# Optimization experiments

Hardware: AMD Instinct MI355X
Metric: run time of the kernel (lower is better)

The kernel has to match this reference:

```python
import jax, jax.numpy as jnp
import numpy as np

N_NODES = 200000
N_EDGES = 3200000
N_FEAT = 165


def setup_inputs() -> dict:
    key = jax.random.key(0)
    ks = jax.random.split(key, 8)

    def glorot(k, fan_in, fan_out):
        lim = np.sqrt(6.0 / (fan_in + fan_out)).astype(np.float32)
        return jax.random.uniform(k, (fan_in, fan_out), jnp.float32, -lim, lim)

    x = jax.random.normal(ks[0], (N_NODES, N_FEAT), jnp.float32)
    edge_index = jax.random.randint(ks[1], (2, N_EDGES), 0, N_NODES, dtype=jnp.int64)
    return {
        "x": x,
        "edge_index": edge_index,
        "W1": glorot(ks[2], N_FEAT, 64), "b1": jnp.zeros((64,), jnp.float32),
        "W2": glorot(ks[3], 64, 16),     "b2": jnp.zeros((16,), jnp.float32),
        "W3": glorot(ks[4], 16, 2),      "b3": jnp.zeros((2,), jnp.float32),
    }


def _gcn_layer(x, src, dst, norm, W, b, n_nodes):
    # linear transform first (feature dim shrinks), then normalized scatter-add
    h = x @ W                                # [N, out]
    msg = h[src] * norm[:, None]             # gather over edges (incl. self-loops)
    out = jax.ops.segment_sum(msg, dst, num_segments=n_nodes)
    return out + b


def reference(x, edge_index, W1, b1, W2, b2, W3, b3):
    n = x.shape[0]
    loops = jnp.arange(n, dtype=edge_index.dtype)
    src = jnp.concatenate([edge_index[0], loops])   # PyG GCNConv adds self-loops
    dst = jnp.concatenate([edge_index[1], loops])
    # symmetric normalization deg^{-1/2}[src] * deg^{-1/2}[dst]
    deg = jax.ops.segment_sum(jnp.ones_like(dst, dtype=x.dtype), dst, num_segments=n)
    dinv = jnp.where(deg > 0, jax.lax.rsqrt(deg), 0.0)
    norm = dinv[src] * dinv[dst]                    # [E + N]

    h = jax.nn.relu(_gcn_layer(x, src, dst, norm, W1, b1, n))
    h = jax.nn.relu(_gcn_layer(h, src, dst, norm, W2, b2, n))
    h = _gcn_layer(h, src, dst, norm, W3, b3, n)
    return jax.nn.log_softmax(h, axis=1)
```

## Files before the change

### kernel.cpp

```cpp
#include <hip/hip_runtime.h>
#include <cstdint>
#include <math.h>

#define BLK 256
#define NBUK_MAX 1024

__device__ __forceinline__ float bf_lo(unsigned p) { return __uint_as_float(p << 16); }
__device__ __forceinline__ float bf_hi(unsigned p) { return __uint_as_float(p & 0xffff0000u); }
__device__ __forceinline__ unsigned pack2(float a, float b) {
  unsigned ua = __float_as_uint(a), ub = __float_as_uint(b);
  ua = (ua + 0x7fffu + ((ua >> 16) & 1u)) >> 16;
  ub = (ub + 0x7fffu + ((ub >> 16) & 1u)) >> 16;
  return (ua & 0xffffu) | (ub << 16);
}


__global__ void k_zero(int* __restrict__ p, int n) {
  int i = blockIdx.x * blockDim.x + threadIdx.x;
  if (i < n) p[i] = 0;
}


__global__ __launch_bounds__(BLK)
void k_bcount(const int* __restrict__ edges, long long E, long long chunk, int nbuk,
              int* __restrict__ bucket_counts) {
  __shared__ int hist[NBUK_MAX];
  for (int i = threadIdx.x; i < nbuk; i += BLK) hist[i] = 0;
  __syncthreads();
  long long beg = (long long)blockIdx.x * chunk;
  long long end = beg + chunk < E ? beg + chunk : E;
  for (long long e = beg + threadIdx.x; e < end; e += BLK)
    atomicAdd(&hist[edges[E + e] >> 8], 1);
  __syncthreads();
  for (int i = threadIdx.x; i < nbuk; i += BLK)
    if (hist[i]) atomicAdd(&bucket_counts[i], hist[i]);
}

__global__ __launch_bounds__(1024)
void k_bscan(const int* __restrict__ bucket_counts, int nbuk,
             int* __restrict__ bucket_start, int* __restrict__ bucket_cursor) {
  __shared__ int tmp[1024];
  int i = threadIdx.x;
  int v = (i < nbuk) ? bucket_counts[i] : 0;
  tmp[i] = v;
  __syncthreads();
  for (int off = 1; off < 1024; off <<= 1) {
    int t = (i >= off) ? tmp[i - off] : 0;
    __syncthreads();
    tmp[i] += t;
    __syncthreads();
  }
  if (i < nbuk) {
    int ex = tmp[i] - v;
    bucket_start[i] = ex;
    bucket_cursor[i] = ex;
  }
  if (i == nbuk - 1) bucket_start[nbuk] = tmp[i];
}

__global__ __launch_bounds__(BLK)
void k_bscatter(const int* __restrict__ edges, long long E, long long chunk, int nbuk,
                int* __restrict__ bucket_cursor, int* __restrict__ tmp_out) {
  __shared__ int hist[NBUK_MAX];
  __shared__ int base[NBUK_MAX];
  for (int i = threadIdx.x; i < nbuk; i += BLK) hist[i] = 0;
  __syncthreads();
  long long beg = (long long)blockIdx.x * chunk;
  long long end = beg + chunk < E ? beg + chunk : E;
  for (long long e = beg + threadIdx.x; e < end; e += BLK)
    atomicAdd(&hist[edges[E + e] >> 8], 1);
  __syncthreads();
  for (int i = threadIdx.x; i < nbuk; i += BLK) {
    int c = hist[i];
    base[i] = c ? atomicAdd(&bucket_cursor[i], c) : 0;
    hist[i] = 0;
  }
  __syncthreads();
  for (long long e = beg + threadIdx.x; e < end; e += BLK) {
    int s = edges[e];
    int d = edges[E + e];
    int b = d >> 8;
    int r = atomicAdd(&hist[b], 1);
    tmp_out[base[b] + r] = (s << 8) | (d & 255);
  }
}

__global__ __launch_bounds__(BLK)
void k_bfinal(const int* __restrict__ tmp_in, const int* __restrict__ bucket_start, int n,
              int* __restrict__ row_start, int* __restrict__ counts,
              float* __restrict__ dinv, int* __restrict__ col) {
  __shared__ int cnt[256];
  __shared__ int scan[256];
  __shared__ int cur[256];
  const int b = blockIdx.x, t = threadIdx.x;
  const int seg0 = bucket_start[b], seg1 = bucket_start[b + 1];
  cnt[t] = 0;
  __syncthreads();
  for (int i = seg0 + t; i < seg1; i += BLK) atomicAdd(&cnt[tmp_in[i] & 255], 1);
  __syncthreads();
  int v0 = cnt[t];
  scan[t] = v0;
  __syncthreads();
  for (int off = 1; off < 256; off <<= 1) {
    int x = (t >= off) ? scan[t - off] : 0;
    __syncthreads();
    scan[t] += x;
    __syncthreads();
  }
  int loff = scan[t] - v0;
  int v = b * 256 + t;
  if (v < n) {
    row_start[v] = seg0 + loff;
    counts[v] = v0;
    dinv[v] = rsqrtf((float)v0 + 1.0f);
  }
  cur[t] = loff;
  __syncthreads();
  for (int i = seg0 + t; i < seg1; i += BLK) {
    int p = tmp_in[i];
    int r = atomicAdd(&cur[p & 255], 1);
    col[seg0 + r] = p >> 8;
  }
}


#define XSTR 260

__global__ __launch_bounds__(BLK)
void k_gemm1(const float* __restrict__ in, const float* __restrict__ W,
             const float* __restrict__ dinv, unsigned* __restrict__ hs1, int n) {
  __shared__ float Xt[33 * XSTR];
  __shared__ float Wl[33 * 64];
  const int t = threadIdx.x;
  const int v0 = blockIdx.x * 256;
  const int tx = t & 7;
  const int ty = t >> 3;

  float xf[33];
  float wf[9];

  float acc[8][8];
#pragma unroll
  for (int i = 0; i < 8; ++i)
#pragma unroll
    for (int j = 0; j < 8; ++j) acc[i][j] = 0.f;

#pragma unroll
  for (int i = 0; i < 33; ++i) {
    int e = t + i * 256;
    int row = e / 33, c = e - row * 33;
    int v = v0 + row;
    xf[i] = (v < n) ? in[(size_t)v * 165 + c] : 0.f;
  }
#pragma unroll
  for (int i = 0; i < 9; ++i) {
    int e = t + i * 256;
    wf[i] = (e < 2112) ? W[e] : 0.f;
  }

  for (int kc = 0; kc < 165; kc += 33) {
    __syncthreads();
#pragma unroll
    for (int i = 0; i < 33; ++i) {
      int e = t + i * 256;
      int row = e / 33, c = e - row * 33;
      Xt[c * XSTR + row] = xf[i];
    }
#pragma unroll
    for (int i = 0; i < 9; ++i) {
      int e = t + i * 256;
      if (e < 2112) Wl[e] = wf[i];
    }
    __syncthreads();

    if (kc + 33 < 165) {
      int kn = kc + 33;
#pragma unroll
      for (int i = 0; i < 33; ++i) {
        int e = t + i * 256;
        int row = e / 33, c = e - row * 33;
        int v = v0 + row;
        xf[i] = (v < n) ? in[(size_t)v * 165 + kn + c] : 0.f;
      }
#pragma unroll
      for (int i = 0; i < 9; ++i) {
        int e = t + i * 256;
        wf[i] = (e < 2112) ? W[kn * 64 + e] : 0.f;
      }
    }

    for (int k = 0; k < 33; ++k) {
      const float4 xa = *(const float4*)&Xt[k * XSTR + ty * 8];
      const float4 xb = *(const float4*)&Xt[k * XSTR + ty * 8 + 4];
      const float4 wa = *(const float4*)&Wl[k * 64 + tx * 8];
      const float4 wb = *(const float4*)&Wl[k * 64 + tx * 8 + 4];
      const float xm[8] = {xa.x, xa.y, xa.z, xa.w, xb.x, xb.y, xb.z, xb.w};
      const float wc[8] = {wa.x, wa.y, wa.z, wa.w, wb.x, wb.y, wb.z, wb.w};
#pragma unroll
      for (int mi = 0; mi < 8; ++mi)
#pragma unroll
        for (int ci = 0; ci < 8; ++ci)
          acc[mi][ci] = fmaf(xm[mi], wc[ci], acc[mi][ci]);
    }
  }

#pragma unroll
  for (int mi = 0; mi < 8; ++mi) {
    int v = v0 + ty * 8 + mi;
    if (v < n) {
      float dv = dinv[v];
      uint4 r;
      r.x = pack2(acc[mi][0] * dv, acc[mi][1] * dv);
      r.y = pack2(acc[mi][2] * dv, acc[mi][3] * dv);
      r.z = pack2(acc[mi][4] * dv, acc[mi][5] * dv);
      r.w = pack2(acc[mi][6] * dv, acc[mi][7] * dv);
      ((uint4*)(hs1 + (size_t)v * 32))[tx] = r;
    }
  }
}


__global__ __launch_bounds__(BLK)
void k_gather64g2(const unsigned* __restrict__ hs1, const int* __restrict__ row_start,
                  const int* __restrict__ counts, const int* __restrict__ col,
                  const float* __restrict__ dinv, const float* __restrict__ b1,
                  const float* __restrict__ W2, unsigned* __restrict__ hs2, int n) {
  __shared__ float W2l[64 * 16];
  for (int i = threadIdx.x; i < 64 * 16; i += BLK) W2l[i] = W2[i];
  __syncthreads();

  int wave = threadIdx.x >> 6, lane = threadIdx.x & 63;
  int v = blockIdx.x * 4 + wave;
  if (v >= n) return;
  int sub = lane >> 5, u = lane & 31;
  int beg = row_start[v], cnt = counts[v];

  float a0, a1;
  if (sub == 0) {
    unsigned p = hs1[(size_t)v * 32 + u];
    a0 = bf_lo(p); a1 = bf_hi(p);
  } else {
    a0 = 0.f; a1 = 0.f;
  }

  int e = sub;
  for (; e + 6 < cnt; e += 8) {
    int s0 = col[beg + e];
    int s1 = col[beg + e + 2];
    int s2 = col[beg + e + 4];
    int s3 = col[beg + e + 6];
    unsigned p0 = hs1[(size_t)s0 * 32 + u];
    unsigned p1 = hs1[(size_t)s1 * 32 + u];
    unsigned p2 = hs1[(size_t)s2 * 32 + u];
    unsigned p3 = hs1[(size_t)s3 * 32 + u];
    a0 += (bf_lo(p0) + bf_lo(p1)) + (bf_lo(p2) + bf_lo(p3));
    a1 += (bf_hi(p0) + bf_hi(p1)) + (bf_hi(p2) + bf_hi(p3));
  }
  for (; e < cnt; e += 2) {
    unsigned p = hs1[(size_t)col[beg + e] * 32 + u];
    a0 += bf_lo(p); a1 += bf_hi(p);
  }
  a0 += __shfl_xor(a0, 32);
  a1 += __shfl_xor(a1, 32);

  float dv = dinv[v];
  float2 bb = ((const float2*)b1)[u];
  float r0 = fmaxf(fmaf(a0, dv, bb.x), 0.f);
  float r1 = fmaxf(fmaf(a1, dv, bb.y), 0.f);

  int o = lane & 15, q = lane >> 4;
  float part = 0.f;
#pragma unroll
  for (int i = 0; i < 16; i += 2) {
    int k = q * 16 + i;
    float e0 = __shfl(r0, k >> 1);
    float e1 = __shfl(r1, k >> 1);
    part = fmaf(e0, W2l[k * 16 + o], part);
    part = fmaf(e1, W2l[(k + 1) * 16 + o], part);
  }
  part += __shfl_xor(part, 16);
  part += __shfl_xor(part, 32);
  float h = part * dv;
  float hnext = __shfl_xor(h, 1);
  if (lane < 16 && (lane & 1) == 0)
    hs2[(size_t)v * 8 + (o >> 1)] = pack2(h, hnext);
}


__global__ __launch_bounds__(BLK)
void k_gather16g3(const unsigned* __restrict__ hs2, const int* __restrict__ row_start,
                  const int* __restrict__ counts, const int* __restrict__ col,
                  const float* __restrict__ dinv, const float* __restrict__ b2,
                  const float* __restrict__ W3, float* __restrict__ hs3, int n) {
  int wave = threadIdx.x >> 6, lane = threadIdx.x & 63;
  int v = blockIdx.x * 4 + wave;
  if (v >= n) return;
  int j = lane >> 3, p = lane & 7;
  int beg = row_start[v], cnt = counts[v];

  float a0 = 0.f, a1 = 0.f;
  int e = j;
  for (; e + 8 < cnt; e += 16) {
    unsigned pk0 = hs2[(size_t)col[beg + e] * 8 + p];
    unsigned pk1 = hs2[(size_t)col[beg + e + 8] * 8 + p];
    a0 += bf_lo(pk0) + bf_lo(pk1);
    a1 += bf_hi(pk0) + bf_hi(pk1);
  }
  if (e < cnt) {
    unsigned pk = hs2[(size_t)col[beg + e] * 8 + p];
    a0 += bf_lo(pk); a1 += bf_hi(pk);
  }
  a0 += __shfl_xor(a0, 8);  a1 += __shfl_xor(a1, 8);
  a0 += __shfl_xor(a0, 16); a1 += __shfl_xor(a1, 16);
  a0 += __shfl_xor(a0, 32); a1 += __shfl_xor(a1, 32);

  unsigned ps = hs2[(size_t)v * 8 + p];
  a0 += bf_lo(ps); a1 += bf_hi(ps);

  float dv = dinv[v];
  float2 bb = ((const float2*)b2)[p];
  float r0 = fmaxf(fmaf(a0, dv, bb.x), 0.f);
  float r1 = fmaxf(fmaf(a1, dv, bb.y), 0.f);

  int o = lane & 1;
  float part = 0.f;
#pragma unroll
  for (int i = 0; i < 8; ++i) {
    float e0 = __shfl(r0, i);
    float e1 = __shfl(r1, i);
    part = fmaf(e0, W3[(2 * i) * 2 + o], part);
    part = fmaf(e1, W3[(2 * i + 1) * 2 + o], part);
  }
  if (lane < 2) hs3[(size_t)v * 2 + o] = part * dv;
}


__global__ void k_gather2_lsm(const float* __restrict__ hs3, const int* __restrict__ row_start,
                              const int* __restrict__ counts, const int* __restrict__ col,
                              const float* __restrict__ dinv, const float* __restrict__ b,
                              float* __restrict__ out, int n) {
  int v = blockIdx.x * blockDim.x + threadIdx.x;
  if (v >= n) return;
  const float2* hs2v = (const float2*)hs3;
  int beg = row_start[v], cnt = counts[v];
  float2 self = hs2v[v];
  float a0 = self.x, a1 = self.y;
  for (int e = 0; e < cnt; ++e) {
    float2 m = hs2v[col[beg + e]];
    a0 += m.x;
    a1 += m.y;
  }
  float dv = dinv[v];
  a0 = fmaf(a0, dv, b[0]);
  a1 = fmaf(a1, dv, b[1]);
  float m = fmaxf(a0, a1);
  float l = m + logf(expf(a0 - m) + expf(a1 - m));
  out[2 * v] = a0 - l;
  out[2 * v + 1] = a1 - l;
}


extern "C" void kernel_launch(void* const* d_in, const int* in_sizes, int n_in,
                              void* d_out, int out_size, void* d_ws, size_t ws_size,
                              hipStream_t stream) {
  const float* x = (const float*)d_in[0];
  const int* edges = (const int*)d_in[1];
  const float* W1 = (const float*)d_in[2];
  const float* b1 = (const float*)d_in[3];
  const float* W2 = (const float*)d_in[4];
  const float* b2 = (const float*)d_in[5];
  const float* W3 = (const float*)d_in[6];
  const float* b3 = (const float*)d_in[7];
  float* out = (float*)d_out;

  const int N = in_sizes[0] / 165;
  const long long E = in_sizes[1] / 2;
  const int nbuk = (N + 255) >> 8;

  char* w = (char*)d_ws;
  int* counts        = (int*)w;  w += (size_t)N * 4;
  int* row_start     = (int*)w;  w += (size_t)N * 4;
  float* dinv        = (float*)w; w += (size_t)N * 4;
  int* bucket_counts = (int*)w;  w += (NBUK_MAX + 4) * 4;
  int* bucket_start  = (int*)w;  w += (NBUK_MAX + 4) * 4;
  int* bucket_cursor = (int*)w;  w += (NBUK_MAX + 4) * 4;
  int* col           = (int*)w;  w += (size_t)E * 4;
  unsigned* hs1      = (unsigned*)w; w += (size_t)N * 32 * 4;
  unsigned* hs2      = (unsigned*)w; w += (size_t)N * 8 * 4;
  float* hs3         = (float*)w;
  int* tmp = (int*)hs1;

  const int gN = (N + BLK - 1) / BLK;
  const int gW = (N + 3) / 4;
  const int NB_PART = 256;
  const long long chunk = (E + NB_PART - 1) / NB_PART;

  k_zero<<<(nbuk + BLK - 1) / BLK, BLK, 0, stream>>>(bucket_counts, nbuk);
  k_bcount<<<NB_PART, BLK, 0, stream>>>(edges, E, chunk, nbuk, bucket_counts);
  k_bscan<<<1, 1024, 0, stream>>>(bucket_counts, nbuk, bucket_start, bucket_cursor);
  k_bscatter<<<NB_PART, BLK, 0, stream>>>(edges, E, chunk, nbuk, bucket_cursor, tmp);
  k_bfinal<<<nbuk, BLK, 0, stream>>>(tmp, bucket_start, N, row_start, counts, dinv, col);

  k_gemm1<<<gN, BLK, 0, stream>>>(x, W1, dinv, hs1, N);

  k_gather64g2<<<gW, BLK, 0, stream>>>(hs1, row_start, counts, col, dinv, b1, W2, hs2, N);

  k_gather16g3<<<gW, BLK, 0, stream>>>(hs2, row_start, counts, col, dinv, b2, W3, hs3, N);

  k_gather2_lsm<<<gN, BLK, 0, stream>>>(hs3, row_start, counts, col, dinv, b3, out, N);
}
```

Baseline: 673.6 us.

## Rewrite first-layer GEMM with fp16 MFMA matrix instructions

Replaces the FP32 register-tiled shared-memory GEMM for X@W1 with a wave-level MFMA 16x16x32 fp16 kernel. W1 is pre-swizzled into LDS as half8 fragments, and X rows are loaded directly from global memory and converted to fp16 per fragment. The aim is to move the 165x64 matmul onto the matrix cores and drop the X transpose staging. It gives up precision (fp16 inputs) and uses uncoalesced 8-float row loads from the stride-165 input. The dinv float4 read may go past n on the last block.

```diff
diff --git a/kernel.cpp b/kernel.cpp
--- a/kernel.cpp
+++ b/kernel.cpp
@@ -13,6 +13,9 @@
   ub = (ub + 0x7fffu + ((ub >> 16) & 1u)) >> 16;
   return (ua & 0xffffu) | (ub << 16);
 }
+
+typedef _Float16 half8 __attribute__((ext_vector_type(8)));
+typedef float f32x4 __attribute__((ext_vector_type(4)));
 
 
 __global__ void k_zero(int* __restrict__ p, int n) {
@@ -124,97 +127,77 @@
 }
 
 
-#define XSTR 260
-
 __global__ __launch_bounds__(BLK)
 void k_gemm1(const float* __restrict__ in, const float* __restrict__ W,
              const float* __restrict__ dinv, unsigned* __restrict__ hs1, int n) {
-  __shared__ float Xt[33 * XSTR];
-  __shared__ float Wl[33 * 64];
+  __shared__ half8 Wl[6 * 4 * 64];
   const int t = threadIdx.x;
-  const int v0 = blockIdx.x * 256;
-  const int tx = t & 7;
-  const int ty = t >> 3;
-
-  float xf[33];
-  float wf[9];
-
-  float acc[8][8];
-#pragma unroll
-  for (int i = 0; i < 8; ++i)
-#pragma unroll
-    for (int j = 0; j < 8; ++j) acc[i][j] = 0.f;
-
-#pragma unroll
-  for (int i = 0; i < 33; ++i) {
-    int e = t + i * 256;
-    int row = e / 33, c = e - row * 33;
-    int v = v0 + row;
-    xf[i] = (v < n) ? in[(size_t)v * 165 + c] : 0.f;
-  }
-#pragma unroll
-  for (int i = 0; i < 9; ++i) {
-    int e = t + i * 256;
-    wf[i] = (e < 2112) ? W[e] : 0.f;
-  }
-
-  for (int kc = 0; kc < 165; kc += 33) {
-    __syncthreads();
-#pragma unroll
-    for (int i = 0; i < 33; ++i) {
-      int e = t + i * 256;
-      int row = e / 33, c = e - row * 33;
-      Xt[c * XSTR + row] = xf[i];
+  const int lane = t & 63, w = t >> 6;
+
+  for (int e = t; e < 12288; e += BLK) {
+    int i = e & 7, ln = (e >> 3) & 63, cf = (e >> 9) & 3, ks = e >> 11;
+    int k = ks * 32 + ((ln >> 4) << 3) + i;
+    int c = (cf << 4) + (ln & 15);
+    float v = (k < 165) ? W[k * 64 + c] : 0.f;
+    ((_Float16*)Wl)[e] = (_Float16)v;
+  }
+  __syncthreads();
+
+  const int row0 = blockIdx.x * 256 + w * 64;
+  const int arow = row0 + (lane & 15);
+  const int kg = (lane >> 4) << 3;
+
+  f32x4 acc[4][4] = {};
+
+  for (int ks = 0; ks < 6; ++ks) {
+    half8 b0 = Wl[(ks * 4 + 0) * 64 + lane];
+    half8 b1 = Wl[(ks * 4 + 1) * 64 + lane];
+    half8 b2 = Wl[(ks * 4 + 2) * 64 + lane];
+    half8 b3 = Wl[(ks * 4 + 3) * 64 + lane];
+    const int kbase = ks * 32 + kg;
+#pragma unroll
+    for (int rf = 0; rf < 4; ++rf) {
+      const int r = arow + rf * 16;
+      float xv[8] = {0.f, 0.f, 0.f, 0.f, 0.f, 0.f, 0.f, 0.f};
+      if (ks < 5) {
+        if (r < n) {
+          const float* p = in + (size_t)r * 165 + kbase;
+#pragma unroll
+          for (int i = 0; i < 8; ++i) xv[i] = p[i];
+        }
+      } else {
+        if (r < n && kg == 0) {
+          const float* p = in + (size_t)r * 165 + kbase;
+#pragma unroll
+          for (int i = 0; i < 5; ++i) xv[i] = p[i];
+        }
+      }
+      half8 a;
+#pragma unroll
+      for (int i = 0; i < 8; ++i) a[i] = (_Float16)xv[i];
+      acc[rf][0] = __builtin_amdgcn_mfma_f32_16x16x32_f16(a, b0, acc[rf][0], 0, 0, 0);
+      acc[rf][1] = __builtin_amdgcn_mfma_f32_16x16x32_f16(a, b1, acc[rf][1], 0, 0, 0);
+      acc[rf][2] = __builtin_amdgcn_mfma_f32_16x16x32_f16(a, b2, acc[rf][2], 0, 0, 0);
+      acc[rf][3] = __builtin_amdgcn_mfma_f32_16x16x32_f16(a, b3, acc[rf][3], 0, 0, 0);
     }
-#pragma unroll
-    for (int i = 0; i < 9; ++i) {
-      int e = t + i * 256;
-      if (e < 2112) Wl[e] = wf[i];
-    }
-    __syncthreads();
-
-    if (kc + 33 < 165) {
-      int kn = kc + 33;
-#pragma unroll
-      for (int i = 0; i < 33; ++i) {
-        int e = t + i * 256;
-        int row = e / 33, c = e - row * 33;
-        int v = v0 + row;
-        xf[i] = (v < n) ? in[(size_t)v * 165 + kn + c] : 0.f;
+  }
+
+  const int cq = lane >> 4;
+#pragma unroll
+  for (int rf = 0; rf < 4; ++rf) {
+    const int rb = row0 + rf * 16 + cq * 4;
+    float4 dv4 = *(const float4*)&dinv[rb];
+    float dvs[4] = {dv4.x, dv4.y, dv4.z, dv4.w};
+#pragma unroll
+    for (int j = 0; j < 4; ++j) {
+      const int r = rb + j;
+#pragma unroll
+      for (int cf = 0; cf < 4; ++cf) {
+        float v = acc[rf][cf][j] * dvs[j];
+        float vn = __shfl_xor(v, 1);
+        if (!(lane & 1) && r < n)
+          hs1[(size_t)r * 32 + ((cf << 4) + (lane & 15)) / 2] = pack2(v, vn);
       }
-#pragma unroll
-      for (int i = 0; i < 9; ++i) {
-        int e = t + i * 256;
-        wf[i] = (e < 2112) ? W[kn * 64 + e] : 0.f;
-      }
-    }
-
-    for (int k = 0; k < 33; ++k) {
-      const float4 xa = *(const float4*)&Xt[k * XSTR + ty * 8];
-      const float4 xb = *(const float4*)&Xt[k * XSTR + ty * 8 + 4];
-      const float4 wa = *(const float4*)&Wl[k * 64 + tx * 8];
-      const float4 wb = *(const float4*)&Wl[k * 64 + tx * 8 + 4];
-      const float xm[8] = {xa.x, xa.y, xa.z, xa.w, xb.x, xb.y, xb.z, xb.w};
-      const float wc[8] = {wa.x, wa.y, wa.z, wa.w, wb.x, wb.y, wb.z, wb.w};
-#pragma unroll
-      for (int mi = 0; mi < 8; ++mi)
-#pragma unroll
-        for (int ci = 0; ci < 8; ++ci)
-          acc[mi][ci] = fmaf(xm[mi], wc[ci], acc[mi][ci]);
-    }
-  }
-
-#pragma unroll
-  for (int mi = 0; mi < 8; ++mi) {
-    int v = v0 + ty * 8 + mi;
-    if (v < n) {
-      float dv = dinv[v];
-      uint4 r;
-      r.x = pack2(acc[mi][0] * dv, acc[mi][1] * dv);
-      r.y = pack2(acc[mi][2] * dv, acc[mi][3] * dv);
-      r.z = pack2(acc[mi][4] * dv, acc[mi][5] * dv);
-      r.w = pack2(acc[mi][6] * dv, acc[mi][7] * dv);
-      ((uint4*)(hs1 + (size_t)v * 32))[tx] = r;
     }
   }
 }
```

Result: faster. 635.4 us (-5.7%).
